# Kernel optimization log

Measured on AMD Instinct MI355X. Metric: run time of the kernel, lower is better.

## Reference

```python
import jax, jax.numpy as jnp
import numpy as np

NEG_SLOPE = 0.2  # PyG GATConv default leaky_relu slope
EPS = 1e-16      # PyG softmax denominator epsilon


def _add_self_loops(edge_index, n):
    loop = jnp.arange(n, dtype=edge_index.dtype)
    src = jnp.concatenate([edge_index[0], loop])
    dst = jnp.concatenate([edge_index[1], loop])
    return src, dst


def _gat_conv(x, src, dst, W, att_src, att_dst, bias, heads, out_ch, n):
    # Linear transform: [N, H, C]
    h = (x @ W).reshape(n, heads, out_ch)
    # Per-node attention logits: [N, H]
    a_s = (h * att_src[None]).sum(-1)
    a_d = (h * att_dst[None]).sum(-1)
    # Edge logits (message j->i uses src term of j, dst term of i): [E, H]
    e = jax.nn.leaky_relu(a_s[src] + a_d[dst], negative_slope=NEG_SLOPE)
    # Segment softmax over incoming edges of each target node
    m = jax.ops.segment_max(e, dst, num_segments=n)  # [N, H]
    ex = jnp.exp(e - m[dst])
    denom = jax.ops.segment_sum(ex, dst, num_segments=n)  # [N, H]
    alpha = ex / (denom[dst] + EPS)  # [E, H]
    # Weighted scatter-aggregate of source features: [N, H, C]
    out = jax.ops.segment_sum(h[src] * alpha[:, :, None], dst, num_segments=n)
    return out, alpha


def setup_inputs() -> dict:
    key = jax.random.key(0)
    ks = jax.random.split(key, 11)
    N, E, IN, HID, HEADS, OUT = 50000, 800000, 128, 64, 3, 64
    g = lambda k, shp, fan: jax.random.normal(k, shp, jnp.float32) * (1.0 / np.sqrt(fan))
    return {
        "x": jax.random.normal(ks[0], (N, IN), jnp.float32),
        "edge_index": jax.random.randint(ks[1], (2, E), 0, N, jnp.int32),
        "W1": g(ks[2], (IN, HEADS * HID), IN),
        "att_src1": g(ks[3], (HEADS, HID), HID),
        "att_dst1": g(ks[4], (HEADS, HID), HID),
        "b1": jnp.zeros((HEADS * HID,), jnp.float32),
        "W2": g(ks[5], (HEADS * HID, OUT), HEADS * HID),
        "att_src2": g(ks[6], (1, OUT), OUT),
        "att_dst2": g(ks[7], (1, OUT), OUT),
        "b2": jnp.zeros((OUT,), jnp.float32),
    }


def reference(x, edge_index, W1, att_src1, att_dst1, b1, W2, att_src2, att_dst2, b2):
    n = x.shape[0]
    heads, hid = att_src1.shape
    out_ch = att_src2.shape[1]
    src, dst = _add_self_loops(edge_index, n)
    # Layer 1: heads concatenated, then bias and ELU
    h1, _alpha = _gat_conv(x, src, dst, W1, att_src1, att_dst1, b1, heads, hid, n)
    h1 = h1.reshape(n, heads * hid) + b1
    h1 = jax.nn.elu(h1)
    # Layer 2: single head (self-loops re-added on same graph, as PyG does)
    h2, _ = _gat_conv(h1, src, dst, W2, att_src2, att_dst2, b2, 1, out_ch, n)
    h2 = h2.reshape(n, out_ch) + b2
    return h2
```

## Files before the change

kernel.cpp:

```cpp
#include <hip/hip_runtime.h>
#include <hip/hip_bf16.h>
#include <cstddef>

#define LRELU_SLOPE 0.2f
#define EPS_DEN 1e-16f

typedef __attribute__((ext_vector_type(8))) short short8;
typedef __attribute__((ext_vector_type(4))) float f32x4;
typedef __attribute__((ext_vector_type(4))) int i32x4;
typedef __attribute__((ext_vector_type(2))) int i32x2;
typedef __attribute__((ext_vector_type(2))) unsigned int u32x2;

__device__ __forceinline__ float lrelu(float v) { return v > 0.f ? v : LRELU_SLOPE * v; }
__device__ __forceinline__ unsigned short f2bf(float f) {
  unsigned int x = __float_as_uint(f);
  unsigned int r = x + 0x7fff + ((x >> 16) & 1);
  return (unsigned short)(r >> 16);
}
__device__ __forceinline__ float lo16(unsigned int u) { return __uint_as_float(u << 16); }
__device__ __forceinline__ float hi16(unsigned int u) { return __uint_as_float(u & 0xffff0000u); }
__device__ __forceinline__ unsigned int pack2(float a, float b) {
  return (unsigned int)f2bf(a) | ((unsigned int)f2bf(b) << 16);
}

template <int K, int NC>
__global__ __launch_bounds__(256) void pack_w_k(const float* __restrict__ W,
                                                unsigned short* __restrict__ Pb) {
  constexpr int CT = NC / 16;
  int t = blockIdx.x * 256 + threadIdx.x;
  constexpr int TOTAL = (K / 32) * CT * 64;
  if (t >= TOTAL) return;
  int lane = t & 63;
  int slot = t >> 6;
  int ct = slot % CT;
  int kt = slot / CT;
  int col = ct * 16 + (lane & 15);
  int kbase = kt * 32 + (lane >> 4) * 8;
  unsigned short v[8];
#pragma unroll
  for (int j = 0; j < 8; ++j) v[j] = f2bf(W[(size_t)(kbase + j) * NC + col]);
#pragma unroll
  for (int j = 0; j < 8; ++j) Pb[(size_t)t * 8 + j] = v[j];
}

template <int K, int NC, bool AF32>
__global__ __launch_bounds__(256) void gemm_mfma_k(const void* __restrict__ Araw,
                                                   const unsigned short* __restrict__ Pb,
                                                   unsigned short* __restrict__ Cb,
                                                   const float* __restrict__ asrc,
                                                   const float* __restrict__ adst,
                                                   float* __restrict__ a_s,
                                                   float* __restrict__ a_d, int M) {
  constexpr int KT = K / 32;
  constexpr int CT = NC / 16;
  constexpr int HEADS = NC / 64;
  const int wv = threadIdx.x >> 6, lane = threadIdx.x & 63;
  const int row0 = blockIdx.x * 64 + wv * 16;
  const int arow = row0 + (lane & 15);
  const int ko = (lane >> 4) * 8;
  const bool aOK = arow < M;

  f32x4 acc[CT];
#pragma unroll
  for (int c = 0; c < CT; ++c) acc[c] = (f32x4){0.f, 0.f, 0.f, 0.f};

#pragma unroll
  for (int kt = 0; kt < KT; ++kt) {
    short8 af;
    if (aOK) {
      if constexpr (AF32) {
        const float* ap = (const float*)Araw + (size_t)arow * K + kt * 32 + ko;
        float4 v0 = *reinterpret_cast<const float4*>(ap);
        float4 v1 = *reinterpret_cast<const float4*>(ap + 4);
        af = (short8){(short)f2bf(v0.x), (short)f2bf(v0.y), (short)f2bf(v0.z), (short)f2bf(v0.w),
                      (short)f2bf(v1.x), (short)f2bf(v1.y), (short)f2bf(v1.z), (short)f2bf(v1.w)};
      } else {
        const unsigned short* ap = (const unsigned short*)Araw + (size_t)arow * K + kt * 32 + ko;
        af = *reinterpret_cast<const short8*>(ap);
      }
    } else {
      af = (short8){0, 0, 0, 0, 0, 0, 0, 0};
    }
#pragma unroll
    for (int ct = 0; ct < CT; ++ct) {
      short8 bf = *reinterpret_cast<const short8*>(Pb + (((size_t)kt * CT + ct) * 64 + lane) * 8);
      acc[ct] = __builtin_amdgcn_mfma_f32_16x16x32_bf16(af, bf, acc[ct], 0, 0, 0);
    }
  }

  float ps[4][HEADS], pd[4][HEADS];
#pragma unroll
  for (int g = 0; g < 4; ++g)
#pragma unroll
    for (int h = 0; h < HEADS; ++h) { ps[g][h] = 0.f; pd[g][h] = 0.f; }
#pragma unroll
  for (int ct = 0; ct < CT; ++ct) {
    int h = ct >> 2;
    float av = asrc[ct * 16 + (lane & 15)];
    float dv = adst[ct * 16 + (lane & 15)];
#pragma unroll
    for (int g = 0; g < 4; ++g) {
      ps[g][h] = fmaf(acc[ct][g], av, ps[g][h]);
      pd[g][h] = fmaf(acc[ct][g], dv, pd[g][h]);
    }
  }
#pragma unroll
  for (int o = 1; o < 16; o <<= 1) {
#pragma unroll
    for (int g = 0; g < 4; ++g)
#pragma unroll
      for (int h = 0; h < HEADS; ++h) {
        ps[g][h] += __shfl_xor(ps[g][h], o);
        pd[g][h] += __shfl_xor(pd[g][h], o);
      }
  }
  if ((lane & 15) == 0) {
#pragma unroll
    for (int g = 0; g < 4; ++g) {
      int gr = row0 + (lane >> 4) * 4 + g;
      if (gr < M) {
#pragma unroll
        for (int h = 0; h < HEADS; ++h) {
          a_s[(size_t)gr * HEADS + h] = ps[g][h];
          a_d[(size_t)gr * HEADS + h] = pd[g][h];
        }
      }
    }
  }

#pragma unroll
  for (int g = 0; g < 4; ++g) {
    int gr = row0 + (lane >> 4) * 4 + g;
    if (gr < M) {
#pragma unroll
      for (int ct = 0; ct < CT; ++ct) {
        Cb[(size_t)gr * NC + ct * 16 + (lane & 15)] = f2bf(acc[ct][g]);
      }
    }
  }
}

__global__ __launch_bounds__(256) void deg_count_k(const int* __restrict__ ei, int E, int Nn,
                                                   int* __restrict__ deg) {
  int e = blockIdx.x * blockDim.x + threadIdx.x;
  int ET = E + Nn;
  if (e >= ET) return;
  int dst = (e < E) ? ei[E + e] : (e - E);
  atomicAdd(&deg[dst], 1);
}

__global__ __launch_bounds__(256) void scan1_k(const int* __restrict__ deg,
                                               int* __restrict__ loc,
                                               int* __restrict__ bsum, int Nn) {
  __shared__ int part[256];
  int t = threadIdx.x;
  int base = blockIdx.x * 1024 + t * 4;
  int v[4];
  int s = 0;
#pragma unroll
  for (int k = 0; k < 4; ++k) {
    int idx = base + k;
    v[k] = (idx < Nn) ? deg[idx] : 0;
    s += v[k];
  }
  part[t] = s;
  __syncthreads();
  for (int o = 1; o < 256; o <<= 1) {
    int u = (t >= o) ? part[t - o] : 0;
    __syncthreads();
    part[t] += u;
    __syncthreads();
  }
  int run = (t == 0) ? 0 : part[t - 1];
#pragma unroll
  for (int k = 0; k < 4; ++k) {
    int idx = base + k;
    if (idx < Nn) loc[idx] = run;
    run += v[k];
  }
  if (t == 255) bsum[blockIdx.x] = part[255];
}

__global__ __launch_bounds__(64) void scan2_k(int* __restrict__ bsum, int nblk) {
  int t = threadIdx.x;
  int v = (t < nblk) ? bsum[t] : 0;
  for (int o = 1; o < 64; o <<= 1) {
    int u = __shfl_up(v, o);
    if (t >= o) v += u;
  }
  if (t < nblk) bsum[t] = v;
}

__global__ __launch_bounds__(256) void scan3_k(const int* __restrict__ loc,
                                               const int* __restrict__ bsum,
                                               int* __restrict__ off,
                                               int* __restrict__ cursor, int Nn, int ET) {
  int i = blockIdx.x * 256 + threadIdx.x;
  if (i < Nn) {
    int blk = i >> 10;
    int basev = blk ? bsum[blk - 1] : 0;
    int o = loc[i] + basev;
    off[i] = o;
    cursor[i] = o;
  }
  if (i == 0) off[Nn] = ET;
}

__global__ __launch_bounds__(256) void fill_k(const int* __restrict__ ei, int E, int Nn,
                                              int* __restrict__ cursor,
                                              int* __restrict__ srcs,
                                              int* __restrict__ dsts) {
  int e = blockIdx.x * blockDim.x + threadIdx.x;
  int ET = E + Nn;
  if (e >= ET) return;
  int src, dst;
  if (e < E) { src = ei[e]; dst = ei[E + e]; }
  else { src = e - E; dst = e - E; }
  int pos = atomicAdd(&cursor[dst], 1);
  srcs[pos] = src;
  dsts[pos] = dst;
}

__global__ __launch_bounds__(256) void ew1_k(const int* __restrict__ srcs,
                                             const int* __restrict__ dsts,
                                             const float* __restrict__ a_s,
                                             const float* __restrict__ a_d,
                                             i32x4* __restrict__ quad, int ET) {
  int p = blockIdx.x * 256 + threadIdx.x;
  if (p >= ET) return;
  int s = srcs[p], d = dsts[p];
  const float* asp = a_s + (size_t)s * 3;
  const float* adp = a_d + (size_t)d * 3;
  float w0 = __expf(lrelu(asp[0] + adp[0]));
  float w1 = __expf(lrelu(asp[1] + adp[1]));
  float w2 = __expf(lrelu(asp[2] + adp[2]));
  quad[p] = (i32x4){s, __float_as_int(w0), __float_as_int(w1), __float_as_int(w2)};
}

__global__ __launch_bounds__(256) void ew2_k(const int* __restrict__ srcs,
                                             const int* __restrict__ dsts,
                                             const float* __restrict__ a_s,
                                             const float* __restrict__ a_d,
                                             i32x2* __restrict__ pair, int ET) {
  int p = blockIdx.x * 256 + threadIdx.x;
  if (p >= ET) return;
  int s = srcs[p], d = dsts[p];
  float w = __expf(lrelu(a_s[s] + a_d[d]));
  pair[p] = (i32x2){s, __float_as_int(w)};
}

__global__ __launch_bounds__(256) void agg1_k(const unsigned int* __restrict__ Hu,
                                              const i32x4* __restrict__ quad,
                                              const int* __restrict__ off,
                                              const float* __restrict__ bias,
                                              unsigned short* __restrict__ outb, int Nn) {
  int wave = threadIdx.x >> 6, lane = threadIdx.x & 63;
  int node = blockIdx.x * 4 + wave;
  if (node >= Nn) return;
  const bool hiHalf = lane >= 32;
  const int q = lane & 31;
  const bool c16 = q < 16;
  int b = off[node], e = off[node + 1];
  float a0 = 0.f, a1 = 0.f, a2 = 0.f, a3 = 0.f;
  float g0 = 0.f, g1 = 0.f, g2 = 0.f, g3 = 0.f;
  float ts0 = 0.f, ts1 = 0.f, ts2 = 0.f;
  int p = b;
#pragma unroll 2
  for (; p + 2 <= e; p += 2) {
    i32x4 e0 = quad[p];
    i32x4 e1 = quad[p + 1];
    float w00 = __int_as_float(e0.y), w01 = __int_as_float(e0.z), w02 = __int_as_float(e0.w);
    float w10 = __int_as_float(e1.y), w11 = __int_as_float(e1.z), w12 = __int_as_float(e1.w);
    int mysrc = hiHalf ? e1.x : e0.x;
    const u32x2* hp = reinterpret_cast<const u32x2*>(Hu + (size_t)mysrc * 96);
    u32x2 u = hp[q];
    float wA = hiHalf ? (c16 ? w10 : w11) : (c16 ? w00 : w01);
    a0 = fmaf(wA, lo16(u.x), a0); a1 = fmaf(wA, hi16(u.x), a1);
    a2 = fmaf(wA, lo16(u.y), a2); a3 = fmaf(wA, hi16(u.y), a3);
    if (c16) {
      u32x2 v = hp[32 + q];
      float wB = hiHalf ? w12 : w02;
      g0 = fmaf(wB, lo16(v.x), g0); g1 = fmaf(wB, hi16(v.x), g1);
      g2 = fmaf(wB, lo16(v.y), g2); g3 = fmaf(wB, hi16(v.y), g3);
    }
    ts0 += w00 + w10; ts1 += w01 + w11; ts2 += w02 + w12;
  }
  if (p < e) {
    i32x4 e0 = quad[p];
    float w00 = __int_as_float(e0.y), w01 = __int_as_float(e0.z), w02 = __int_as_float(e0.w);
    const u32x2* hp = reinterpret_cast<const u32x2*>(Hu + (size_t)e0.x * 96);
    u32x2 u = hp[q];
    float wA = hiHalf ? 0.f : (c16 ? w00 : w01);
    a0 = fmaf(wA, lo16(u.x), a0); a1 = fmaf(wA, hi16(u.x), a1);
    a2 = fmaf(wA, lo16(u.y), a2); a3 = fmaf(wA, hi16(u.y), a3);
    if (c16) {
      u32x2 v = hp[32 + q];
      float wB = hiHalf ? 0.f : w02;
      g0 = fmaf(wB, lo16(v.x), g0); g1 = fmaf(wB, hi16(v.x), g1);
      g2 = fmaf(wB, lo16(v.y), g2); g3 = fmaf(wB, hi16(v.y), g3);
    }
    ts0 += w00; ts1 += w01; ts2 += w02;
  }
  a0 += __shfl_xor(a0, 32); a1 += __shfl_xor(a1, 32);
  a2 += __shfl_xor(a2, 32); a3 += __shfl_xor(a3, 32);
  g0 += __shfl_xor(g0, 32); g1 += __shfl_xor(g1, 32);
  g2 += __shfl_xor(g2, 32); g3 += __shfl_xor(g3, 32);

  if (!hiHalf) {
    float r = 1.f / ((c16 ? ts0 : ts1) + EPS_DEN);
    int col = 4 * q;
    float o0 = a0 * r + bias[col], o1 = a1 * r + bias[col + 1];
    float o2 = a2 * r + bias[col + 2], o3 = a3 * r + bias[col + 3];
    o0 = o0 > 0.f ? o0 : expm1f(o0);
    o1 = o1 > 0.f ? o1 : expm1f(o1);
    o2 = o2 > 0.f ? o2 : expm1f(o2);
    o3 = o3 > 0.f ? o3 : expm1f(o3);
    u32x2 pk = {pack2(o0, o1), pack2(o2, o3)};
    __builtin_nontemporal_store(pk, reinterpret_cast<u32x2*>(&outb[(size_t)node * 192 + col]));
  } else if (c16) {
    float r = 1.f / (ts2 + EPS_DEN);
    int col = 128 + 4 * q;
    float o0 = g0 * r + bias[col], o1 = g1 * r + bias[col + 1];
    float o2 = g2 * r + bias[col + 2], o3 = g3 * r + bias[col + 3];
    o0 = o0 > 0.f ? o0 : expm1f(o0);
    o1 = o1 > 0.f ? o1 : expm1f(o1);
    o2 = o2 > 0.f ? o2 : expm1f(o2);
    o3 = o3 > 0.f ? o3 : expm1f(o3);
    u32x2 pk = {pack2(o0, o1), pack2(o2, o3)};
    __builtin_nontemporal_store(pk, reinterpret_cast<u32x2*>(&outb[(size_t)node * 192 + col]));
  }
}

__global__ __launch_bounds__(256) void agg2_k(const unsigned int* __restrict__ Hu,
                                              const i32x2* __restrict__ pair,
                                              const int* __restrict__ off,
                                              const float* __restrict__ bias,
                                              float* __restrict__ out, int Nn) {
  int wave = threadIdx.x >> 6, lane = threadIdx.x & 63;
  int node = blockIdx.x * 4 + wave;
  if (node >= Nn) return;
  const int sub = lane >> 4;
  const int l = lane & 15;
  int b = off[node], e = off[node + 1];
  float c0 = 0.f, c1 = 0.f, c2 = 0.f, c3 = 0.f;
  float ts = 0.f;
  int p = b;
  for (; p + 4 <= e; p += 4) {
    i32x2 p0 = pair[p], p1 = pair[p + 1], p2 = pair[p + 2], p3 = pair[p + 3];
    float w0 = __int_as_float(p0.y), w1 = __int_as_float(p1.y);
    float w2 = __int_as_float(p2.y), w3 = __int_as_float(p3.y);
    int mysrc = (sub == 0) ? p0.x : (sub == 1) ? p1.x : (sub == 2) ? p2.x : p3.x;
    float myw = (sub == 0) ? w0 : (sub == 1) ? w1 : (sub == 2) ? w2 : w3;
    const u32x2* hp = reinterpret_cast<const u32x2*>(Hu + (size_t)mysrc * 32);
    u32x2 u = hp[l];
    c0 = fmaf(myw, lo16(u.x), c0); c1 = fmaf(myw, hi16(u.x), c1);
    c2 = fmaf(myw, lo16(u.y), c2); c3 = fmaf(myw, hi16(u.y), c3);
    ts += w0 + w1 + w2 + w3;
  }
  if (p < e) {
    i32x2 p0 = pair[p], p1 = pair[p + 1], p2 = pair[p + 2], p3 = pair[p + 3];
    bool h1 = p + 1 < e, h2 = p + 2 < e, h3 = p + 3 < e;
    float w0 = __int_as_float(p0.y);
    float w1 = h1 ? __int_as_float(p1.y) : 0.f;
    float w2 = h2 ? __int_as_float(p2.y) : 0.f;
    float w3 = h3 ? __int_as_float(p3.y) : 0.f;
    int s0 = p0.x;
    int s1 = h1 ? p1.x : s0, s2 = h2 ? p2.x : s0, s3 = h3 ? p3.x : s0;
    int mysrc = (sub == 0) ? s0 : (sub == 1) ? s1 : (sub == 2) ? s2 : s3;
    float myw = (sub == 0) ? w0 : (sub == 1) ? w1 : (sub == 2) ? w2 : w3;
    const u32x2* hp = reinterpret_cast<const u32x2*>(Hu + (size_t)mysrc * 32);
    u32x2 u = hp[l];
    c0 = fmaf(myw, lo16(u.x), c0); c1 = fmaf(myw, hi16(u.x), c1);
    c2 = fmaf(myw, lo16(u.y), c2); c3 = fmaf(myw, hi16(u.y), c3);
    ts += w0 + w1 + w2 + w3;
  }
  c0 += __shfl_xor(c0, 16); c0 += __shfl_xor(c0, 32);
  c1 += __shfl_xor(c1, 16); c1 += __shfl_xor(c1, 32);
  c2 += __shfl_xor(c2, 16); c2 += __shfl_xor(c2, 32);
  c3 += __shfl_xor(c3, 16); c3 += __shfl_xor(c3, 32);
  if (lane < 16) {
    float r = 1.f / (ts + EPS_DEN);
    int col = 4 * l;
    f32x4 v = {c0 * r + bias[col], c1 * r + bias[col + 1],
               c2 * r + bias[col + 2], c3 * r + bias[col + 3]};
    __builtin_nontemporal_store(v, reinterpret_cast<f32x4*>(&out[(size_t)node * 64 + col]));
  }
}

extern "C" void kernel_launch(void* const* d_in, const int* in_sizes, int n_in,
                              void* d_out, int out_size, void* d_ws, size_t ws_size,
                              hipStream_t stream) {
  const float* x = (const float*)d_in[0];
  const int* ei = (const int*)d_in[1];
  const float* W1 = (const float*)d_in[2];
  const float* att_src1 = (const float*)d_in[3];
  const float* att_dst1 = (const float*)d_in[4];
  const float* b1 = (const float*)d_in[5];
  const float* W2 = (const float*)d_in[6];
  const float* att_src2 = (const float*)d_in[7];
  const float* att_dst2 = (const float*)d_in[8];
  const float* b2 = (const float*)d_in[9];

  const int IN = 128, HEADS = 3;
  const int HC1 = 192;
  const int N = in_sizes[0] / IN;
  const int E = in_sizes[1] / 2;
  const int ET = E + N;
  const int ETp = ET + 4;

  char* base = (char*)d_ws;
  i32x4* quad1 = (i32x4*)base;
  unsigned short* h1_postb = (unsigned short*)(base + (size_t)ETp * 16);
  float* a_s1 = (float*)(h1_postb + (size_t)N * HC1);
  float* a_d1 = a_s1 + (size_t)N * HEADS;
  int* deg = (int*)(a_d1 + (size_t)N * HEADS);
  int* off = deg + N;
  int* cursor = off + (N + 1);
  int* bsum = cursor + N;
  int* srcs = bsum + 256;
  int* dsts = srcs + ET;
  size_t pw_off = ((size_t)((char*)(dsts + ET) - base) + 15) & ~(size_t)15;
  unsigned short* packW1 = (unsigned short*)(base + pw_off);
  unsigned short* packW2 = packW1 + 24576;
  size_t ph_off = ((size_t)((char*)(packW2 + 12288) - base) + 15) & ~(size_t)15;
  char* ph = base + ph_off;
  unsigned short* h1b = (unsigned short*)ph;
  unsigned short* h2b = (unsigned short*)ph;
  i32x2* pair2 = (i32x2*)(ph + (size_t)N * 384);
  float* a_s2 = (float*)((char*)pair2 + (size_t)ETp * 8);
  float* a_d2 = a_s2 + N;

  float* outp = (float*)d_out;

  int gemm_blocks = (N + 63) / 64;
  int row_blocks = (N + 3) / 4;
  int edge_blocks = (ET + 255) / 256;
  int nblk = (N + 1023) / 1024;

  pack_w_k<128, 192><<<12, 256, 0, stream>>>(W1, packW1);
  pack_w_k<192, 64><<<6, 256, 0, stream>>>(W2, packW2);

  hipMemsetAsync(deg, 0, (size_t)N * sizeof(int), stream);
  deg_count_k<<<edge_blocks, 256, 0, stream>>>(ei, E, N, deg);
  scan1_k<<<nblk, 256, 0, stream>>>(deg, cursor, bsum, N);
  scan2_k<<<1, 64, 0, stream>>>(bsum, nblk);
  scan3_k<<<(N + 255) / 256, 256, 0, stream>>>(cursor, bsum, off, cursor, N, ET);
  fill_k<<<edge_blocks, 256, 0, stream>>>(ei, E, N, cursor, srcs, dsts);

  gemm_mfma_k<128, 192, true><<<gemm_blocks, 256, 0, stream>>>(x, packW1, h1b, att_src1,
                                                               att_dst1, a_s1, a_d1, N);
  ew1_k<<<edge_blocks, 256, 0, stream>>>(srcs, dsts, a_s1, a_d1, quad1, ET);
  agg1_k<<<row_blocks, 256, 0, stream>>>((const unsigned int*)h1b, quad1, off, b1,
                                         h1_postb, N);

  gemm_mfma_k<192, 64, false><<<gemm_blocks, 256, 0, stream>>>(h1_postb, packW2, h2b,
                                                               att_src2, att_dst2,
                                                               a_s2, a_d2, N);
  ew2_k<<<edge_blocks, 256, 0, stream>>>(srcs, dsts, a_s2, a_d2, pair2, ET);
  agg2_k<<<row_blocks, 256, 0, stream>>>((const unsigned int*)h2b, pair2, off, b2,
                                         outp, N);

  (void)n_in; (void)out_size; (void)ws_size;
}
```

Measured before the change: 260.9 us.

## Split GAT aggregation into per-head, per-half-channel passes over a 2D grid

Replaces the two node-per-wave aggregation kernels with one templated kernel launched over a 2D grid. Each grid-y slice handles one head and one 32-channel half, so a pass gathers only a 64-byte slice of each source row. The layer-1 edge weights are now stored as per-head (src, weight) pairs instead of 16-byte quads. The aim is a smaller per-pass gather footprint that fits in cache better and more parallelism. In exchange, edge lists and offsets are re-read once per pass (6 for layer 1, 2 for layer 2), the layer-1 edge-weight kernel writes more data, and each lane does less work.

```diff
diff --git a/kernel.cpp b/kernel.cpp
--- a/kernel.cpp
+++ b/kernel.cpp
@@ -7,9 +7,8 @@
 
 typedef __attribute__((ext_vector_type(8))) short short8;
 typedef __attribute__((ext_vector_type(4))) float f32x4;
-typedef __attribute__((ext_vector_type(4))) int i32x4;
 typedef __attribute__((ext_vector_type(2))) int i32x2;
-typedef __attribute__((ext_vector_type(2))) unsigned int u32x2;
+typedef __attribute__((ext_vector_type(2))) float f32x2;
 
 __device__ __forceinline__ float lrelu(float v) { return v > 0.f ? v : LRELU_SLOPE * v; }
 __device__ __forceinline__ unsigned short f2bf(float f) {
@@ -225,7 +224,8 @@
                                              const int* __restrict__ dsts,
                                              const float* __restrict__ a_s,
                                              const float* __restrict__ a_d,
-                                             i32x4* __restrict__ quad, int ET) {
+                                             i32x2* __restrict__ pairsH, int ETstride,
+                                             int ET) {
   int p = blockIdx.x * 256 + threadIdx.x;
   if (p >= ET) return;
   int s = srcs[p], d = dsts[p];
@@ -234,7 +234,9 @@
   float w0 = __expf(lrelu(asp[0] + adp[0]));
   float w1 = __expf(lrelu(asp[1] + adp[1]));
   float w2 = __expf(lrelu(asp[2] + adp[2]));
-  quad[p] = (i32x4){s, __float_as_int(w0), __float_as_int(w1), __float_as_int(w2)};
+  pairsH[p] = (i32x2){s, __float_as_int(w0)};
+  pairsH[(size_t)ETstride + p] = (i32x2){s, __float_as_int(w1)};
+  pairsH[(size_t)2 * ETstride + p] = (i32x2){s, __float_as_int(w2)};
 }
 
 __global__ __launch_bounds__(256) void ew2_k(const int* __restrict__ srcs,
@@ -249,141 +251,65 @@
   pair[p] = (i32x2){s, __float_as_int(w)};
 }
 
-__global__ __launch_bounds__(256) void agg1_k(const unsigned int* __restrict__ Hu,
-                                              const i32x4* __restrict__ quad,
-                                              const int* __restrict__ off,
-                                              const float* __restrict__ bias,
-                                              unsigned short* __restrict__ outb, int Nn) {
+template <int ROWU32, int OUTSTRIDE, bool BF16OUT>
+__global__ __launch_bounds__(256) void agg_pass_k(
+    const unsigned int* __restrict__ Hu,
+    const i32x2* __restrict__ pairs, int ETstride,
+    const int* __restrict__ off,
+    const float* __restrict__ bias,
+    void* __restrict__ outv, int Nn) {
+  const int pass = blockIdx.y;
+  const int head = pass >> 1;
+  const int half = pass & 1;
+  const i32x2* ph = pairs + (size_t)head * ETstride;
+  const int chanU32 = head * 32 + half * 16;
   int wave = threadIdx.x >> 6, lane = threadIdx.x & 63;
   int node = blockIdx.x * 4 + wave;
   if (node >= Nn) return;
-  const bool hiHalf = lane >= 32;
-  const int q = lane & 31;
-  const bool c16 = q < 16;
+  const int sub = lane >> 4, l = lane & 15;
   int b = off[node], e = off[node + 1];
-  float a0 = 0.f, a1 = 0.f, a2 = 0.f, a3 = 0.f;
-  float g0 = 0.f, g1 = 0.f, g2 = 0.f, g3 = 0.f;
-  float ts0 = 0.f, ts1 = 0.f, ts2 = 0.f;
+  float c0 = 0.f, c1 = 0.f, ts = 0.f;
   int p = b;
-#pragma unroll 2
-  for (; p + 2 <= e; p += 2) {
-    i32x4 e0 = quad[p];
-    i32x4 e1 = quad[p + 1];
-    float w00 = __int_as_float(e0.y), w01 = __int_as_float(e0.z), w02 = __int_as_float(e0.w);
-    float w10 = __int_as_float(e1.y), w11 = __int_as_float(e1.z), w12 = __int_as_float(e1.w);
-    int mysrc = hiHalf ? e1.x : e0.x;
-    const u32x2* hp = reinterpret_cast<const u32x2*>(Hu + (size_t)mysrc * 96);
-    u32x2 u = hp[q];
-    float wA = hiHalf ? (c16 ? w10 : w11) : (c16 ? w00 : w01);
-    a0 = fmaf(wA, lo16(u.x), a0); a1 = fmaf(wA, hi16(u.x), a1);
-    a2 = fmaf(wA, lo16(u.y), a2); a3 = fmaf(wA, hi16(u.y), a3);
-    if (c16) {
-      u32x2 v = hp[32 + q];
-      float wB = hiHalf ? w12 : w02;
-      g0 = fmaf(wB, lo16(v.x), g0); g1 = fmaf(wB, hi16(v.x), g1);
-      g2 = fmaf(wB, lo16(v.y), g2); g3 = fmaf(wB, hi16(v.y), g3);
-    }
-    ts0 += w00 + w10; ts1 += w01 + w11; ts2 += w02 + w12;
-  }
-  if (p < e) {
-    i32x4 e0 = quad[p];
-    float w00 = __int_as_float(e0.y), w01 = __int_as_float(e0.z), w02 = __int_as_float(e0.w);
-    const u32x2* hp = reinterpret_cast<const u32x2*>(Hu + (size_t)e0.x * 96);
-    u32x2 u = hp[q];
-    float wA = hiHalf ? 0.f : (c16 ? w00 : w01);
-    a0 = fmaf(wA, lo16(u.x), a0); a1 = fmaf(wA, hi16(u.x), a1);
-    a2 = fmaf(wA, lo16(u.y), a2); a3 = fmaf(wA, hi16(u.y), a3);
-    if (c16) {
-      u32x2 v = hp[32 + q];
-      float wB = hiHalf ? 0.f : w02;
-      g0 = fmaf(wB, lo16(v.x), g0); g1 = fmaf(wB, hi16(v.x), g1);
-      g2 = fmaf(wB, lo16(v.y), g2); g3 = fmaf(wB, hi16(v.y), g3);
-    }
-    ts0 += w00; ts1 += w01; ts2 += w02;
-  }
-  a0 += __shfl_xor(a0, 32); a1 += __shfl_xor(a1, 32);
-  a2 += __shfl_xor(a2, 32); a3 += __shfl_xor(a3, 32);
-  g0 += __shfl_xor(g0, 32); g1 += __shfl_xor(g1, 32);
-  g2 += __shfl_xor(g2, 32); g3 += __shfl_xor(g3, 32);
-
-  if (!hiHalf) {
-    float r = 1.f / ((c16 ? ts0 : ts1) + EPS_DEN);
-    int col = 4 * q;
-    float o0 = a0 * r + bias[col], o1 = a1 * r + bias[col + 1];
-    float o2 = a2 * r + bias[col + 2], o3 = a3 * r + bias[col + 3];
-    o0 = o0 > 0.f ? o0 : expm1f(o0);
-    o1 = o1 > 0.f ? o1 : expm1f(o1);
-    o2 = o2 > 0.f ? o2 : expm1f(o2);
-    o3 = o3 > 0.f ? o3 : expm1f(o3);
-    u32x2 pk = {pack2(o0, o1), pack2(o2, o3)};
-    __builtin_nontemporal_store(pk, reinterpret_cast<u32x2*>(&outb[(size_t)node * 192 + col]));
-  } else if (c16) {
-    float r = 1.f / (ts2 + EPS_DEN);
-    int col = 128 + 4 * q;
-    float o0 = g0 * r + bias[col], o1 = g1 * r + bias[col + 1];
-    float o2 = g2 * r + bias[col + 2], o3 = g3 * r + bias[col + 3];
-    o0 = o0 > 0.f ? o0 : expm1f(o0);
-    o1 = o1 > 0.f ? o1 : expm1f(o1);
-    o2 = o2 > 0.f ? o2 : expm1f(o2);
-    o3 = o3 > 0.f ? o3 : expm1f(o3);
-    u32x2 pk = {pack2(o0, o1), pack2(o2, o3)};
-    __builtin_nontemporal_store(pk, reinterpret_cast<u32x2*>(&outb[(size_t)node * 192 + col]));
-  }
-}
-
-__global__ __launch_bounds__(256) void agg2_k(const unsigned int* __restrict__ Hu,
-                                              const i32x2* __restrict__ pair,
-                                              const int* __restrict__ off,
-                                              const float* __restrict__ bias,
-                                              float* __restrict__ out, int Nn) {
-  int wave = threadIdx.x >> 6, lane = threadIdx.x & 63;
-  int node = blockIdx.x * 4 + wave;
-  if (node >= Nn) return;
-  const int sub = lane >> 4;
-  const int l = lane & 15;
-  int b = off[node], e = off[node + 1];
-  float c0 = 0.f, c1 = 0.f, c2 = 0.f, c3 = 0.f;
-  float ts = 0.f;
-  int p = b;
-  for (; p + 4 <= e; p += 4) {
-    i32x2 p0 = pair[p], p1 = pair[p + 1], p2 = pair[p + 2], p3 = pair[p + 3];
-    float w0 = __int_as_float(p0.y), w1 = __int_as_float(p1.y);
-    float w2 = __int_as_float(p2.y), w3 = __int_as_float(p3.y);
-    int mysrc = (sub == 0) ? p0.x : (sub == 1) ? p1.x : (sub == 2) ? p2.x : p3.x;
-    float myw = (sub == 0) ? w0 : (sub == 1) ? w1 : (sub == 2) ? w2 : w3;
-    const u32x2* hp = reinterpret_cast<const u32x2*>(Hu + (size_t)mysrc * 32);
-    u32x2 u = hp[l];
-    c0 = fmaf(myw, lo16(u.x), c0); c1 = fmaf(myw, hi16(u.x), c1);
-    c2 = fmaf(myw, lo16(u.y), c2); c3 = fmaf(myw, hi16(u.y), c3);
-    ts += w0 + w1 + w2 + w3;
-  }
-  if (p < e) {
-    i32x2 p0 = pair[p], p1 = pair[p + 1], p2 = pair[p + 2], p3 = pair[p + 3];
-    bool h1 = p + 1 < e, h2 = p + 2 < e, h3 = p + 3 < e;
-    float w0 = __int_as_float(p0.y);
-    float w1 = h1 ? __int_as_float(p1.y) : 0.f;
-    float w2 = h2 ? __int_as_float(p2.y) : 0.f;
-    float w3 = h3 ? __int_as_float(p3.y) : 0.f;
-    int s0 = p0.x;
-    int s1 = h1 ? p1.x : s0, s2 = h2 ? p2.x : s0, s3 = h3 ? p3.x : s0;
-    int mysrc = (sub == 0) ? s0 : (sub == 1) ? s1 : (sub == 2) ? s2 : s3;
-    float myw = (sub == 0) ? w0 : (sub == 1) ? w1 : (sub == 2) ? w2 : w3;
-    const u32x2* hp = reinterpret_cast<const u32x2*>(Hu + (size_t)mysrc * 32);
-    u32x2 u = hp[l];
-    c0 = fmaf(myw, lo16(u.x), c0); c1 = fmaf(myw, hi16(u.x), c1);
-    c2 = fmaf(myw, lo16(u.y), c2); c3 = fmaf(myw, hi16(u.y), c3);
-    ts += w0 + w1 + w2 + w3;
+  for (; p + 8 <= e; p += 8) {
+    i32x2 prA = ph[p + sub];
+    i32x2 prB = ph[p + 4 + sub];
+    unsigned int uA = Hu[(size_t)prA.x * ROWU32 + chanU32 + l];
+    unsigned int uB = Hu[(size_t)prB.x * ROWU32 + chanU32 + l];
+    float wA = __int_as_float(prA.y);
+    float wB = __int_as_float(prB.y);
+    c0 = fmaf(wA, lo16(uA), c0); c1 = fmaf(wA, hi16(uA), c1);
+    c0 = fmaf(wB, lo16(uB), c0); c1 = fmaf(wB, hi16(uB), c1);
+    ts += wA + wB;
+  }
+  for (; p < e; p += 4) {
+    int idx = min(p + sub, e - 1);
+    i32x2 pr = ph[idx];
+    float w = (p + sub < e) ? __int_as_float(pr.y) : 0.f;
+    unsigned int u = Hu[(size_t)pr.x * ROWU32 + chanU32 + l];
+    c0 = fmaf(w, lo16(u), c0);
+    c1 = fmaf(w, hi16(u), c1);
+    ts += w;
   }
   c0 += __shfl_xor(c0, 16); c0 += __shfl_xor(c0, 32);
   c1 += __shfl_xor(c1, 16); c1 += __shfl_xor(c1, 32);
-  c2 += __shfl_xor(c2, 16); c2 += __shfl_xor(c2, 32);
-  c3 += __shfl_xor(c3, 16); c3 += __shfl_xor(c3, 32);
+  ts += __shfl_xor(ts, 16); ts += __shfl_xor(ts, 32);
   if (lane < 16) {
     float r = 1.f / (ts + EPS_DEN);
-    int col = 4 * l;
-    f32x4 v = {c0 * r + bias[col], c1 * r + bias[col + 1],
-               c2 * r + bias[col + 2], c3 * r + bias[col + 3]};
-    __builtin_nontemporal_store(v, reinterpret_cast<f32x4*>(&out[(size_t)node * 64 + col]));
+    int col = chanU32 * 2 + 2 * l;
+    float o0 = c0 * r + bias[col];
+    float o1 = c1 * r + bias[col + 1];
+    if constexpr (BF16OUT) {
+      o0 = o0 > 0.f ? o0 : expm1f(o0);
+      o1 = o1 > 0.f ? o1 : expm1f(o1);
+      unsigned int pk = pack2(o0, o1);
+      __builtin_nontemporal_store(
+          pk, reinterpret_cast<unsigned int*>((unsigned short*)outv +
+                                              (size_t)node * OUTSTRIDE + col));
+    } else {
+      f32x2 v = {o0, o1};
+      __builtin_nontemporal_store(
+          v, reinterpret_cast<f32x2*>((float*)outv + (size_t)node * OUTSTRIDE + col));
+    }
   }
 }
 
@@ -406,14 +332,16 @@
   const int N = in_sizes[0] / IN;
   const int E = in_sizes[1] / 2;
   const int ET = E + N;
-  const int ETp = ET + 4;
 
   char* base = (char*)d_ws;
-  i32x4* quad1 = (i32x4*)base;
-  unsigned short* h1_postb = (unsigned short*)(base + (size_t)ETp * 16);
+  i32x2* pairsH1 = (i32x2*)base;
+  i32x2* pair2 = pairsH1 + (size_t)3 * ET;
+  unsigned short* h1_postb = (unsigned short*)(pair2 + ET);
   float* a_s1 = (float*)(h1_postb + (size_t)N * HC1);
   float* a_d1 = a_s1 + (size_t)N * HEADS;
-  int* deg = (int*)(a_d1 + (size_t)N * HEADS);
+  float* a_s2 = a_d1 + (size_t)N * HEADS;
+  float* a_d2 = a_s2 + N;
+  int* deg = (int*)(a_d2 + N);
   int* off = deg + N;
   int* cursor = off + (N + 1);
   int* bsum = cursor + N;
@@ -426,9 +354,6 @@
   char* ph = base + ph_off;
   unsigned short* h1b = (unsigned short*)ph;
   unsigned short* h2b = (unsigned short*)ph;
-  i32x2* pair2 = (i32x2*)(ph + (size_t)N * 384);
-  float* a_s2 = (float*)((char*)pair2 + (size_t)ETp * 8);
-  float* a_d2 = a_s2 + N;
 
   float* outp = (float*)d_out;
 
@@ -449,16 +374,16 @@
 
   gemm_mfma_k<128, 192, true><<<gemm_blocks, 256, 0, stream>>>(x, packW1, h1b, att_src1,
                                                                att_dst1, a_s1, a_d1, N);
-  ew1_k<<<edge_blocks, 256, 0, stream>>>(srcs, dsts, a_s1, a_d1, quad1, ET);
-  agg1_k<<<row_blocks, 256, 0, stream>>>((const unsigned int*)h1b, quad1, off, b1,
-                                         h1_postb, N);
+  ew1_k<<<edge_blocks, 256, 0, stream>>>(srcs, dsts, a_s1, a_d1, pairsH1, ET, ET);
+  agg_pass_k<96, 192, true><<<dim3(row_blocks, 6), 256, 0, stream>>>(
+      (const unsigned int*)h1b, pairsH1, ET, off, b1, h1_postb, N);
 
   gemm_mfma_k<192, 64, false><<<gemm_blocks, 256, 0, stream>>>(h1_postb, packW2, h2b,
                                                                att_src2, att_dst2,
                                                                a_s2, a_d2, N);
   ew2_k<<<edge_blocks, 256, 0, stream>>>(srcs, dsts, a_s2, a_d2, pair2, ET);
-  agg2_k<<<row_blocks, 256, 0, stream>>>((const unsigned int*)h2b, pair2, off, b2,
-                                         outp, N);
+  agg_pass_k<32, 64, false><<<dim3(row_blocks, 2), 256, 0, stream>>>(
+      (const unsigned int*)h2b, pair2, ET, off, b2, outp, N);
 
   (void)n_in; (void)out_size; (void)ws_size;
 }
```

Measured after the change: 339.1 us. 1.3x slower.

## Remap layer-1 aggregation lanes to full-row gathers with four-edge unrolling

Applied to the files above, without the earlier changes.

Changes the lane mapping in the layer-1 aggregation kernel so that every lane of the wave reads one 32-bit word (two bf16 channels) of the first 128 columns for each edge. The third head's 64 columns are split across the two half-waves by edge parity. The edge loop now processes four edges per iteration with more independent gathers in flight, and most cross-half shuffles are removed. The aim is better memory-level parallelism and fewer idle or divergent lanes, at the cost of narrower per-lane loads and somewhat more registers.

```diff
diff --git a/kernel.cpp b/kernel.cpp
--- a/kernel.cpp
+++ b/kernel.cpp
@@ -257,77 +257,111 @@
   int wave = threadIdx.x >> 6, lane = threadIdx.x & 63;
   int node = blockIdx.x * 4 + wave;
   if (node >= Nn) return;
-  const bool hiHalf = lane >= 32;
-  const int q = lane & 31;
-  const bool c16 = q < 16;
+  bool hiHalf = lane >= 32;
+  int q = lane & 31;
   int b = off[node], e = off[node + 1];
-  float a0 = 0.f, a1 = 0.f, a2 = 0.f, a3 = 0.f;
-  float g0 = 0.f, g1 = 0.f, g2 = 0.f, g3 = 0.f;
+  float accAx = 0.f, accAy = 0.f, accBx = 0.f, accBy = 0.f;
   float ts0 = 0.f, ts1 = 0.f, ts2 = 0.f;
   int p = b;
-#pragma unroll 2
+  for (; p + 4 <= e; p += 4) {
+    i32x4 q0 = quad[p];
+    i32x4 q1 = quad[p + 1];
+    i32x4 q2 = quad[p + 2];
+    i32x4 q3 = quad[p + 3];
+    const unsigned int* h0 = Hu + (size_t)q0.x * 96;
+    const unsigned int* h1 = Hu + (size_t)q1.x * 96;
+    const unsigned int* h2 = Hu + (size_t)q2.x * 96;
+    const unsigned int* h3 = Hu + (size_t)q3.x * 96;
+    unsigned int a0 = h0[lane];
+    unsigned int a1 = h1[lane];
+    unsigned int a2 = h2[lane];
+    unsigned int a3 = h3[lane];
+    unsigned int bm0 = (hiHalf ? h1 : h0)[64 + q];
+    unsigned int bm1 = (hiHalf ? h3 : h2)[64 + q];
+    float w00 = __int_as_float(q0.y), w01 = __int_as_float(q0.z), w02 = __int_as_float(q0.w);
+    float w10 = __int_as_float(q1.y), w11 = __int_as_float(q1.z), w12 = __int_as_float(q1.w);
+    float w20 = __int_as_float(q2.y), w21 = __int_as_float(q2.z), w22 = __int_as_float(q2.w);
+    float w30 = __int_as_float(q3.y), w31 = __int_as_float(q3.z), w32 = __int_as_float(q3.w);
+    float wA0 = hiHalf ? w01 : w00;
+    float wA1 = hiHalf ? w11 : w10;
+    float wA2 = hiHalf ? w21 : w20;
+    float wA3 = hiHalf ? w31 : w30;
+    float wB0 = hiHalf ? w12 : w02;
+    float wB1 = hiHalf ? w32 : w22;
+    accAx = fmaf(wA0, lo16(a0), accAx);
+    accAy = fmaf(wA0, hi16(a0), accAy);
+    accAx = fmaf(wA1, lo16(a1), accAx);
+    accAy = fmaf(wA1, hi16(a1), accAy);
+    accAx = fmaf(wA2, lo16(a2), accAx);
+    accAy = fmaf(wA2, hi16(a2), accAy);
+    accAx = fmaf(wA3, lo16(a3), accAx);
+    accAy = fmaf(wA3, hi16(a3), accAy);
+    accBx = fmaf(wB0, lo16(bm0), accBx);
+    accBy = fmaf(wB0, hi16(bm0), accBy);
+    accBx = fmaf(wB1, lo16(bm1), accBx);
+    accBy = fmaf(wB1, hi16(bm1), accBy);
+    ts0 += w00 + w10 + w20 + w30;
+    ts1 += w01 + w11 + w21 + w31;
+    ts2 += w02 + w12 + w22 + w32;
+  }
   for (; p + 2 <= e; p += 2) {
-    i32x4 e0 = quad[p];
-    i32x4 e1 = quad[p + 1];
-    float w00 = __int_as_float(e0.y), w01 = __int_as_float(e0.z), w02 = __int_as_float(e0.w);
-    float w10 = __int_as_float(e1.y), w11 = __int_as_float(e1.z), w12 = __int_as_float(e1.w);
-    int mysrc = hiHalf ? e1.x : e0.x;
-    const u32x2* hp = reinterpret_cast<const u32x2*>(Hu + (size_t)mysrc * 96);
-    u32x2 u = hp[q];
-    float wA = hiHalf ? (c16 ? w10 : w11) : (c16 ? w00 : w01);
-    a0 = fmaf(wA, lo16(u.x), a0); a1 = fmaf(wA, hi16(u.x), a1);
-    a2 = fmaf(wA, lo16(u.y), a2); a3 = fmaf(wA, hi16(u.y), a3);
-    if (c16) {
-      u32x2 v = hp[32 + q];
-      float wB = hiHalf ? w12 : w02;
-      g0 = fmaf(wB, lo16(v.x), g0); g1 = fmaf(wB, hi16(v.x), g1);
-      g2 = fmaf(wB, lo16(v.y), g2); g3 = fmaf(wB, hi16(v.y), g3);
-    }
+    i32x4 q0 = quad[p];
+    i32x4 q1 = quad[p + 1];
+    float w00 = __int_as_float(q0.y), w01 = __int_as_float(q0.z), w02 = __int_as_float(q0.w);
+    float w10 = __int_as_float(q1.y), w11 = __int_as_float(q1.z), w12 = __int_as_float(q1.w);
+    const unsigned int* h0 = Hu + (size_t)q0.x * 96;
+    const unsigned int* h1 = Hu + (size_t)q1.x * 96;
+    unsigned int a0 = h0[lane];
+    unsigned int bm = (hiHalf ? h1 : h0)[64 + q];
+    unsigned int a1 = h1[lane];
+    float wA0 = hiHalf ? w01 : w00;
+    float wA1 = hiHalf ? w11 : w10;
+    float wB = hiHalf ? w12 : w02;
+    accAx = fmaf(wA0, lo16(a0), accAx);
+    accAy = fmaf(wA0, hi16(a0), accAy);
+    accAx = fmaf(wA1, lo16(a1), accAx);
+    accAy = fmaf(wA1, hi16(a1), accAy);
+    accBx = fmaf(wB, lo16(bm), accBx);
+    accBy = fmaf(wB, hi16(bm), accBy);
     ts0 += w00 + w10; ts1 += w01 + w11; ts2 += w02 + w12;
   }
   if (p < e) {
-    i32x4 e0 = quad[p];
-    float w00 = __int_as_float(e0.y), w01 = __int_as_float(e0.z), w02 = __int_as_float(e0.w);
-    const u32x2* hp = reinterpret_cast<const u32x2*>(Hu + (size_t)e0.x * 96);
-    u32x2 u = hp[q];
-    float wA = hiHalf ? 0.f : (c16 ? w00 : w01);
-    a0 = fmaf(wA, lo16(u.x), a0); a1 = fmaf(wA, hi16(u.x), a1);
-    a2 = fmaf(wA, lo16(u.y), a2); a3 = fmaf(wA, hi16(u.y), a3);
-    if (c16) {
-      u32x2 v = hp[32 + q];
-      float wB = hiHalf ? 0.f : w02;
-      g0 = fmaf(wB, lo16(v.x), g0); g1 = fmaf(wB, hi16(v.x), g1);
-      g2 = fmaf(wB, lo16(v.y), g2); g3 = fmaf(wB, hi16(v.y), g3);
-    }
+    i32x4 q0 = quad[p];
+    float w00 = __int_as_float(q0.y), w01 = __int_as_float(q0.z), w02 = __int_as_float(q0.w);
+    const unsigned int* h0 = Hu + (size_t)q0.x * 96;
+    unsigned int a0 = h0[lane];
+    unsigned int bm = h0[64 + q];
+    float wA0 = hiHalf ? w01 : w00;
+    float wB = hiHalf ? 0.f : w02;
+    accAx = fmaf(wA0, lo16(a0), accAx);
+    accAy = fmaf(wA0, hi16(a0), accAy);
+    accBx = fmaf(wB, lo16(bm), accBx);
+    accBy = fmaf(wB, hi16(bm), accBy);
     ts0 += w00; ts1 += w01; ts2 += w02;
   }
-  a0 += __shfl_xor(a0, 32); a1 += __shfl_xor(a1, 32);
-  a2 += __shfl_xor(a2, 32); a3 += __shfl_xor(a3, 32);
-  g0 += __shfl_xor(g0, 32); g1 += __shfl_xor(g1, 32);
-  g2 += __shfl_xor(g2, 32); g3 += __shfl_xor(g3, 32);
-
-  if (!hiHalf) {
-    float r = 1.f / ((c16 ? ts0 : ts1) + EPS_DEN);
-    int col = 4 * q;
-    float o0 = a0 * r + bias[col], o1 = a1 * r + bias[col + 1];
-    float o2 = a2 * r + bias[col + 2], o3 = a3 * r + bias[col + 3];
-    o0 = o0 > 0.f ? o0 : expm1f(o0);
-    o1 = o1 > 0.f ? o1 : expm1f(o1);
-    o2 = o2 > 0.f ? o2 : expm1f(o2);
-    o3 = o3 > 0.f ? o3 : expm1f(o3);
-    u32x2 pk = {pack2(o0, o1), pack2(o2, o3)};
-    __builtin_nontemporal_store(pk, reinterpret_cast<u32x2*>(&outb[(size_t)node * 192 + col]));
-  } else if (c16) {
-    float r = 1.f / (ts2 + EPS_DEN);
-    int col = 128 + 4 * q;
-    float o0 = g0 * r + bias[col], o1 = g1 * r + bias[col + 1];
-    float o2 = g2 * r + bias[col + 2], o3 = g3 * r + bias[col + 3];
-    o0 = o0 > 0.f ? o0 : expm1f(o0);
-    o1 = o1 > 0.f ? o1 : expm1f(o1);
-    o2 = o2 > 0.f ? o2 : expm1f(o2);
-    o3 = o3 > 0.f ? o3 : expm1f(o3);
-    u32x2 pk = {pack2(o0, o1), pack2(o2, o3)};
-    __builtin_nontemporal_store(pk, reinterpret_cast<u32x2*>(&outb[(size_t)node * 192 + col]));
+  accBx += __shfl_xor(accBx, 32);
+  accBy += __shfl_xor(accBy, 32);
+
+  float tsA = hiHalf ? ts1 : ts0;
+  float rA = 1.f / (tsA + EPS_DEN);
+  float rB = 1.f / (ts2 + EPS_DEN);
+  int colA = (hiHalf ? 64 : 0) + 2 * q;
+  float oA0 = accAx * rA + bias[colA];
+  float oA1 = accAy * rA + bias[colA + 1];
+  oA0 = oA0 > 0.f ? oA0 : expm1f(oA0);
+  oA1 = oA1 > 0.f ? oA1 : expm1f(oA1);
+  unsigned int pkA = pack2(oA0, oA1);
+  __builtin_nontemporal_store(
+      pkA, reinterpret_cast<unsigned int*>(&outb[(size_t)node * 192 + colA]));
+  if (hiHalf) {
+    int colB = 128 + 2 * q;
+    float oB0 = accBx * rB + bias[colB];
+    float oB1 = accBy * rB + bias[colB + 1];
+    oB0 = oB0 > 0.f ? oB0 : expm1f(oB0);
+    oB1 = oB1 > 0.f ? oB1 : expm1f(oB1);
+    unsigned int pkB = pack2(oB0, oB1);
+    __builtin_nontemporal_store(
+        pkB, reinterpret_cast<unsigned int*>(&outb[(size_t)node * 192 + colB]));
   }
 }
 
```

After: 247.1 us. -5.3%, faster.
